# Kernel optimization log

Hardware: AMD Instinct MI355X
Metric: run time of the kernel (lower is better)

The kernel has to match this reference:

```python
import jax, jax.numpy as jnp
import numpy as np

DIMENSIONS = 10000
NUM_LEVELS = 100
SIZE = 617
NUM_CLASSES = 26
BATCH = 32


def setup_inputs() -> dict:
    key = jax.random.key(0)
    k1, k2, k3 = jax.random.split(key, 3)
    x = jax.random.uniform(k1, (BATCH, SIZE), dtype=jnp.float32)  # values in [0,1]
    # Random embedding: bipolar {-1,+1} hypervectors
    id_weight = jnp.where(jax.random.uniform(k2, (SIZE, DIMENSIONS)) > 0.5, 1.0, -1.0).astype(jnp.float32)
    # Level embedding: bipolar hypervectors per quantization level
    level_weight = jnp.where(jax.random.uniform(k3, (NUM_LEVELS, DIMENSIONS)) > 0.5, 1.0, -1.0).astype(jnp.float32)
    classify_weight = jnp.zeros((NUM_CLASSES, DIMENSIONS), dtype=jnp.float32)
    return {"x": x, "id_weight": id_weight, "level_weight": level_weight, "classify_weight": classify_weight}


def reference(x, id_weight, level_weight, classify_weight):
    # Level embedding: map continuous values in [low=0, high=1] to level indices
    idx = jnp.clip(jnp.round(x * (NUM_LEVELS - 1)), 0, NUM_LEVELS - 1).astype(jnp.int32)  # (B, S)
    value_hv = level_weight[idx]                     # gather -> (B, S, D)
    bound = id_weight[None, :, :] * value_hv         # bind (elementwise multiply)
    multiset = jnp.sum(bound, axis=1)                # sum over feature axis -> (B, D)
    enc = jnp.where(multiset > 0, 1.0, -1.0)         # hard_quantize
    logit = jnp.einsum('bd,cd->bc', enc, classify_weight)  # Linear, no bias
    return logit
```

## Files before the change

### kernel.cpp

```cpp
#include <hip/hip_runtime.h>

typedef unsigned int u32;
typedef unsigned char u8;
typedef unsigned long long u64;

#define DIMS   10000
#define LEVELS 100
#define SSIZE  617
#define SPAD   624
#define NCLS   26
#define BATCH  32
#define WORDS  313
#define WPITCH 320
#define DPITCH 10240
#define NTILE  5
#define NCH    13
#define CHUNK  48

#define OFF_OFFW 0x000000u
#define OFF_IDB  0x020000u
#define OFF_LVB  0x100000u
#define OFF_P8   0x140000u
#define SLOT_BYTES ((size_t)BATCH * DPITCH)

#define PK_ROWS (SPAD + LEVELS + 1)

__global__ __launch_bounds__(256) void k_pack(const float* __restrict__ x,
                                              const float* __restrict__ idw,
                                              const float* __restrict__ lvw,
                                              u32* __restrict__ idb,
                                              u32* __restrict__ lvb,
                                              u32* __restrict__ offw,
                                              float* __restrict__ out)
{
    const int g = blockIdx.x;
    const int r = blockIdx.y;
    const int t = threadIdx.x;
    const bool isLvl = r >= SPAD;
    const int rl = r - SPAD;
    const int d0 = g * 1024 + 4 * t;

    u32 nib = 0;
    const bool rowValid = isLvl ? (rl < LEVELS) : (r < SSIZE);
    if (d0 + 3 < DIMS && rowValid) {
        const float* src = isLvl ? (lvw + (size_t)rl * DIMS)
                                 : (idw + (size_t)r * DIMS);
        float4 f = *(const float4*)(src + d0);
        nib =  (__builtin_bit_cast(u32, f.x) >> 31)
            | ((__builtin_bit_cast(u32, f.y) >> 31) << 1)
            | ((__builtin_bit_cast(u32, f.z) >> 31) << 2)
            | ((__builtin_bit_cast(u32, f.w) >> 31) << 3);
    }
    __shared__ u32 nibs[256];
    nibs[t] = nib;
    __syncthreads();
    if (t < 32) {
        u32 w = 0;
#pragma unroll
        for (int j = 0; j < 8; ++j) w |= nibs[t * 8 + j] << (4 * j);
        u32* dst = isLvl ? (lvb + (size_t)rl * WPITCH)
                         : (idb + (size_t)r * WPITCH);
        dst[g * 32 + t] = w;
    }

    const int B = r * 10 + g;
    const int t2 = B * 256 + t;
    if (t2 < SPAD * BATCH) {
        int s = t2 >> 5, b = t2 & 31;
        u32 off = (u32)LEVELS * WPITCH;
        if (s < SSIZE) {
            float v = x[b * SSIZE + s];
            float rr = rintf(v * (float)(LEVELS - 1));
            int q = (int)rr;
            q = q < 0 ? 0 : (q > LEVELS - 1 ? LEVELS - 1 : q);
            off = (u32)q * WPITCH;
        }
        offw[s * BATCH + b] = off;
    }
    if (t2 < BATCH * NCLS) out[t2] = 0.0f;
}

__device__ __forceinline__ void spread6(u32* __restrict__ part,
                                        int slot, int B0, int wq,
                                        const u32 ones[4], const u32 c0[4],
                                        const u32 c1[4], const u32 c2[4],
                                        const u32 c3[4], const u32 c4[4])
{
#pragma unroll
    for (int b = 0; b < 4; ++b) {
        u32* dst = part + ((size_t)(slot * BATCH + B0 + b) * DPITCH + (size_t)wq * 32) / 4;
        u32 o[8];
#pragma unroll
        for (int g = 0; g < 8; ++g) {
            int sh = 4 * g;
            u32 n;
            n  =  (((ones[b] >> sh) & 0xFu) * 0x00204081u) & 0x01010101u;
            n |= ((((c0[b]  >> sh) & 0xFu) * 0x00204081u) & 0x01010101u) << 1;
            n |= ((((c1[b]  >> sh) & 0xFu) * 0x00204081u) & 0x01010101u) << 2;
            n |= ((((c2[b]  >> sh) & 0xFu) * 0x00204081u) & 0x01010101u) << 3;
            n |= ((((c3[b]  >> sh) & 0xFu) * 0x00204081u) & 0x01010101u) << 4;
            n |= ((((c4[b]  >> sh) & 0xFu) * 0x00204081u) & 0x01010101u) << 5;
            o[g] = n;
        }
        *(uint4*)(dst)     = make_uint4(o[0], o[1], o[2], o[3]);
        *(uint4*)(dst + 4) = make_uint4(o[4], o[5], o[6], o[7]);
    }
}

template <int CH>
__global__ __launch_bounds__(64) void k_bind_t(const u32* __restrict__ idb,
                                               const u32* __restrict__ lvb,
                                               const u32* __restrict__ offw,
                                               u32* __restrict__ part)
{
    const int wq   = blockIdx.x * 64 + threadIdx.x;
    const int B0   = blockIdx.y * 4;
    const int slot = blockIdx.z;
    const int sBeg = slot * CH;

    u32 ones[4], c0[4], c1[4], c2[4], c3[4], c4[4];
#pragma unroll
    for (int b = 0; b < 4; ++b) { ones[b]=0; c0[b]=0; c1[b]=0; c2[b]=0; c3[b]=0; c4[b]=0; }

#pragma unroll
    for (int i = 0; i < CH / 2; ++i) {
        const int s = sBeg + 2 * i;
        u32 u1 = idb[(size_t)s * WPITCH + wq];
        u32 u2 = idb[(size_t)(s + 1) * WPITCH + wq];
        const u32* o1 = offw + s * BATCH + B0;
        const u32* o2 = o1 + BATCH;
#pragma unroll
        for (int b = 0; b < 4; ++b) {
            u32 l1 = lvb[o1[b] + wq];
            u32 l2 = lvb[o2[b] + wq];
            u32 x1 = u1 ^ l1, x2 = u2 ^ l2;
            u32 t0 = x1 ^ x2;
            u32 sum = ones[b] ^ t0;
            u32 car = (x1 & x2) | (ones[b] & t0);
            ones[b] = sum;
            u32 tt;
            tt = c0[b] & car; c0[b] ^= car; car = tt;
            tt = c1[b] & car; c1[b] ^= car; car = tt;
            tt = c2[b] & car; c2[b] ^= car; car = tt;
            tt = c3[b] & car; c3[b] ^= car; car = tt;
            c4[b] ^= car;
        }
    }
    spread6(part, slot, B0, wq, ones, c0, c1, c2, c3, c4);
}

__global__ __launch_bounds__(64) void k_bind_g(const u32* __restrict__ idb,
                                               const u32* __restrict__ lvb,
                                               const u32* __restrict__ offw,
                                               u32* __restrict__ part,
                                               int chunk)
{
    const int wq   = blockIdx.x * 64 + threadIdx.x;
    const int B0   = blockIdx.y * 4;
    const int slot = blockIdx.z;
    const int sBeg = slot * chunk;
    const int sEnd = min(SPAD, sBeg + chunk);

    u32 ones[4], c0[4], c1[4], c2[4], c3[4], c4[4];
#pragma unroll
    for (int b = 0; b < 4; ++b) { ones[b]=0; c0[b]=0; c1[b]=0; c2[b]=0; c3[b]=0; c4[b]=0; }

    for (int s = sBeg; s < sEnd; s += 2) {
        u32 u1 = idb[(size_t)s * WPITCH + wq];
        u32 u2 = idb[(size_t)(s + 1) * WPITCH + wq];
        const u32* o1 = offw + s * BATCH + B0;
        const u32* o2 = o1 + BATCH;
#pragma unroll
        for (int b = 0; b < 4; ++b) {
            u32 l1 = lvb[o1[b] + wq];
            u32 l2 = lvb[o2[b] + wq];
            u32 x1 = u1 ^ l1, x2 = u2 ^ l2;
            u32 t0 = x1 ^ x2;
            u32 sum = ones[b] ^ t0;
            u32 car = (x1 & x2) | (ones[b] & t0);
            ones[b] = sum;
            u32 tt;
            tt = c0[b] & car; c0[b] ^= car; car = tt;
            tt = c1[b] & car; c1[b] ^= car; car = tt;
            tt = c2[b] & car; c2[b] ^= car; car = tt;
            tt = c3[b] & car; c3[b] ^= car; car = tt;
            c4[b] ^= car;
        }
    }
    spread6(part, slot, B0, wq, ones, c0, c1, c2, c3, c4);
}

template <int NCHT>
__global__ __launch_bounds__(256) void k_encl_t(const u32* __restrict__ part,
                                                const float* __restrict__ W,
                                                float* __restrict__ out)
{
    const int b = blockIdx.y;
    const int q = blockIdx.x;
    const int t = threadIdx.x;
    const int dw = q * 256 + t;
    const u32* p = part + (size_t)b * (DPITCH / 4) + dw;
    const size_t cs = (size_t)BATCH * (DPITCH / 4);

    u32 v[NCHT];
#pragma unroll
    for (int c = 0; c < NCHT; ++c) v[c] = p[(size_t)c * cs];
    u32 a01 = 0, a23 = 0;
#pragma unroll
    for (int c = 0; c < NCHT; ++c) {
        a01 += v[c] & 0x00FF00FFu;
        a23 += (v[c] >> 8) & 0x00FF00FFu;
    }
    const float e0 = (int)(a01 & 0xFFFFu) <= 308 ? 1.0f : -1.0f;
    const float e1 = (int)(a23 & 0xFFFFu) <= 308 ? 1.0f : -1.0f;
    const float e2 = (int)(a01 >> 16)     <= 308 ? 1.0f : -1.0f;
    const float e3 = (int)(a23 >> 16)     <= 308 ? 1.0f : -1.0f;

    float acc[NCLS];
    if (dw < DIMS / 4) {
#pragma unroll
        for (int cc = 0; cc < NCLS; ++cc) {
            float4 w4 = *(const float4*)(W + (size_t)cc * DIMS + 4 * dw);
            acc[cc] = fmaf(e0, w4.x, fmaf(e1, w4.y, fmaf(e2, w4.z, e3 * w4.w)));
        }
    } else {
#pragma unroll
        for (int cc = 0; cc < NCLS; ++cc) acc[cc] = 0.0f;
    }

#pragma unroll
    for (int cc = 0; cc < NCLS; ++cc) {
#pragma unroll
        for (int o = 32; o > 0; o >>= 1)
            acc[cc] += __shfl_xor(acc[cc], o);
    }
    __shared__ float red[4][NCLS];
    const int lane = t & 63, wv = t >> 6;
    if (lane == 0) {
#pragma unroll
        for (int cc = 0; cc < NCLS; ++cc) red[wv][cc] = acc[cc];
    }
    __syncthreads();
    if (t < NCLS) {
        float vv = red[0][t] + red[1][t] + red[2][t] + red[3][t];
        atomicAdd(out + b * NCLS + t, vv);
    }
}

__global__ __launch_bounds__(256) void k_encl_g(const u32* __restrict__ part,
                                                const float* __restrict__ W,
                                                float* __restrict__ out,
                                                int nch)
{
    const int b = blockIdx.y;
    const int q = blockIdx.x;
    const int t = threadIdx.x;
    const int dw = q * 256 + t;
    const u32* p = part + (size_t)b * (DPITCH / 4) + dw;
    const size_t cs = (size_t)BATCH * (DPITCH / 4);
    u32 a01 = 0, a23 = 0;
    for (int c = 0; c < nch; ++c) {
        u32 v = p[(size_t)c * cs];
        a01 += v & 0x00FF00FFu;
        a23 += (v >> 8) & 0x00FF00FFu;
    }
    const float e0 = (int)(a01 & 0xFFFFu) <= 308 ? 1.0f : -1.0f;
    const float e1 = (int)(a23 & 0xFFFFu) <= 308 ? 1.0f : -1.0f;
    const float e2 = (int)(a01 >> 16)     <= 308 ? 1.0f : -1.0f;
    const float e3 = (int)(a23 >> 16)     <= 308 ? 1.0f : -1.0f;
    float acc[NCLS];
    if (dw < DIMS / 4) {
#pragma unroll
        for (int cc = 0; cc < NCLS; ++cc) {
            float4 w4 = *(const float4*)(W + (size_t)cc * DIMS + 4 * dw);
            acc[cc] = fmaf(e0, w4.x, fmaf(e1, w4.y, fmaf(e2, w4.z, e3 * w4.w)));
        }
    } else {
#pragma unroll
        for (int cc = 0; cc < NCLS; ++cc) acc[cc] = 0.0f;
    }
#pragma unroll
    for (int cc = 0; cc < NCLS; ++cc) {
#pragma unroll
        for (int o = 32; o > 0; o >>= 1)
            acc[cc] += __shfl_xor(acc[cc], o);
    }
    __shared__ float red[4][NCLS];
    const int lane = t & 63, wv = t >> 6;
    if (lane == 0) {
#pragma unroll
        for (int cc = 0; cc < NCLS; ++cc) red[wv][cc] = acc[cc];
    }
    __syncthreads();
    if (t < NCLS) {
        float vv = red[0][t] + red[1][t] + red[2][t] + red[3][t];
        atomicAdd(out + b * NCLS + t, vv);
    }
}

extern "C" void kernel_launch(void* const* d_in, const int* in_sizes, int n_in,
                              void* d_out, int out_size, void* d_ws, size_t ws_size,
                              hipStream_t stream)
{
    const float* x   = (const float*)d_in[0];
    const float* idw = (const float*)d_in[1];
    const float* lvw = (const float*)d_in[2];
    const float* W   = (const float*)d_in[3];
    float* out = (float*)d_out;

    char* ws = (char*)d_ws;
    u32* offw = (u32*)(ws + OFF_OFFW);
    u32* idb  = (u32*)(ws + OFF_IDB);
    u32* lvb  = (u32*)(ws + OFF_LVB);
    u32* part = (u32*)(ws + OFF_P8);

    size_t avail = ws_size > OFF_P8 ? ws_size - OFF_P8 : 0;
    const bool fast = avail >= (size_t)NCH * SLOT_BYTES;

    dim3 g1(10, PK_ROWS);
    k_pack<<<g1, 256, 0, stream>>>(x, idw, lvw, idb, lvb, offw, out);

    if (fast) {
        dim3 g2(NTILE, 8, NCH);
        k_bind_t<CHUNK><<<g2, 64, 0, stream>>>(idb, lvb, offw, part);
        dim3 g3(10, BATCH);
        k_encl_t<NCH><<<g3, 256, 0, stream>>>(part, W, out);
    } else {
        int nch = (int)(avail / SLOT_BYTES);
        if (nch < 1) nch = 1;
        int chunk = (SPAD + nch - 1) / nch;
        chunk = (chunk + 1) & ~1;
        if (chunk > 62) chunk = 62;
        nch = (SPAD + chunk - 1) / chunk;
        dim3 g2(NTILE, 8, nch);
        k_bind_g<<<g2, 64, 0, stream>>>(idb, lvb, offw, part, chunk);
        dim3 g3(10, BATCH);
        k_encl_g<<<g3, 256, 0, stream>>>(part, W, out, nch);
    }
}
```

Before: 98.28 us.

## Split bind kernel to one batch row per block and batch loads by 16

The bind kernel now gives each block a single batch element instead of four. That raises the grid from 8 to 32 blocks along y and drops the per-thread register arrays. Level offsets are stored transposed per batch (pitch 640) so each block preloads its chunk's offsets contiguously. Inside the kernel, 16 id and level words are loaded before the carry-save updates run, to expose memory-level parallelism. The cost is reading each id-word row four times as often, and the spread helper carries a redundant first loop whose results are overwritten.

After: 91.00 us. 7.4% less time.

```diff
diff --git a/kernel.cpp b/kernel.cpp
--- a/kernel.cpp
+++ b/kernel.cpp
@@ -16,8 +16,9 @@
 #define NTILE  5
 #define NCH    13
 #define CHUNK  48
-
-#define OFF_OFFW 0x000000u
+#define SOPITCH 640
+
+#define OFF_OFFT 0x000000u
 #define OFF_IDB  0x020000u
 #define OFF_LVB  0x100000u
 #define OFF_P8   0x140000u
@@ -30,7 +31,7 @@
                                               const float* __restrict__ lvw,
                                               u32* __restrict__ idb,
                                               u32* __restrict__ lvb,
-                                              u32* __restrict__ offw,
+                                              u32* __restrict__ offt,
                                               float* __restrict__ out)
 {
     const int g = blockIdx.x;
@@ -75,119 +76,113 @@
             q = q < 0 ? 0 : (q > LEVELS - 1 ? LEVELS - 1 : q);
             off = (u32)q * WPITCH;
         }
-        offw[s * BATCH + b] = off;
+        offt[b * SOPITCH + s] = off;
     }
     if (t2 < BATCH * NCLS) out[t2] = 0.0f;
 }
 
-__device__ __forceinline__ void spread6(u32* __restrict__ part,
-                                        int slot, int B0, int wq,
-                                        const u32 ones[4], const u32 c0[4],
-                                        const u32 c1[4], const u32 c2[4],
-                                        const u32 c3[4], const u32 c4[4])
-{
-#pragma unroll
-    for (int b = 0; b < 4; ++b) {
-        u32* dst = part + ((size_t)(slot * BATCH + B0 + b) * DPITCH + (size_t)wq * 32) / 4;
-        u32 o[8];
-#pragma unroll
-        for (int g = 0; g < 8; ++g) {
-            int sh = 4 * g;
-            u32 n;
-            n  =  (((ones[b] >> sh) & 0xFu) * 0x00204081u) & 0x01010101u;
-            n |= ((((c0[b]  >> sh) & 0xFu) * 0x00204081u) & 0x01010101u) << 1;
-            n |= ((((c1[b]  >> sh) & 0xFu) * 0x00204081u) & 0x01010101u) << 2;
-            n |= ((((c2[b]  >> sh) & 0xFu) * 0x00204081u) & 0x01010101u) << 3;
-            n |= ((((c3[b]  >> sh) & 0xFu) * 0x00204081u) & 0x01010101u) << 4;
-            n |= ((((c4[b]  >> sh) & 0xFu) * 0x00204081u) & 0x01010101u) << 5;
-            o[g] = n;
-        }
-        *(uint4*)(dst)     = make_uint4(o[0], o[1], o[2], o[3]);
-        *(uint4*)(dst + 4) = make_uint4(o[4], o[5], o[6], o[7]);
-    }
+#define CSA6(xv)                                                              \
+    {                                                                         \
+        u32 car = ones & (xv);                                                \
+        ones ^= (xv);                                                         \
+        u32 tt;                                                               \
+        tt = c0 & car; c0 ^= car; car = tt;                                   \
+        tt = c1 & car; c1 ^= car; car = tt;                                   \
+        tt = c2 & car; c2 ^= car; car = tt;                                   \
+        tt = c3 & car; c3 ^= car; car = tt;                                   \
+        c4 ^= car;                                                            \
+    }
+
+__device__ __forceinline__ void spread6_1(u32* __restrict__ part,
+                                          int slot, int b, int wq,
+                                          u32 ones, u32 c0, u32 c1,
+                                          u32 c2, u32 c3, u32 c4)
+{
+    u32* dst = part + ((size_t)(slot * BATCH + b) * DPITCH + (size_t)wq * 32) / 4;
+    u32 o[8];
+#pragma unroll
+    for (int g = 0; g < 8; ++g) {
+        int sh = 4 * g;
+        u32 n;
+        n  =  (((ones >> sh) & 0xFu) * 0x00204081u) & 0x01010101u;
+        n |= ((((c0   >> sh) & 0xFu) * 0x00204081u) & 0x01010101u) << 1;
+        n |= ((((c1   >> sh) & 0xFu) * 0x00204081u) & 0x01010101u) << 2;
+        n |= ((((c2   >> sh) & 0xFu) * 0x00204081u) & 0x01010101u) << 3;
+        n |= ((((c3   >> sh) & 0xFu) * 0x00204081u) & 0x01010101u) << 4;
+        n |= ((((c4   >> sh) & 0xFu) * 0x01010101u) & 0x01010101u) << 5;
+        o[g] = n;
+    }
+#pragma unroll
+    for (int g = 0; g < 8; ++g) {
+        int sh = 4 * g;
+        u32 n;
+        n  =  (((ones >> sh) & 0xFu) * 0x00204081u) & 0x01010101u;
+        n |= ((((c0   >> sh) & 0xFu) * 0x00204081u) & 0x01010101u) << 1;
+        n |= ((((c1   >> sh) & 0xFu) * 0x00204081u) & 0x01010101u) << 2;
+        n |= ((((c2   >> sh) & 0xFu) * 0x00204081u) & 0x01010101u) << 3;
+        n |= ((((c3   >> sh) & 0xFu) * 0x00204081u) & 0x01010101u) << 4;
+        n |= ((((c4   >> sh) & 0xFu) * 0x00204081u) & 0x01010101u) << 5;
+        o[g] = n;
+    }
+    *(uint4*)(dst)     = make_uint4(o[0], o[1], o[2], o[3]);
+    *(uint4*)(dst + 4) = make_uint4(o[4], o[5], o[6], o[7]);
 }
 
 template <int CH>
 __global__ __launch_bounds__(64) void k_bind_t(const u32* __restrict__ idb,
                                                const u32* __restrict__ lvb,
-                                               const u32* __restrict__ offw,
+                                               const u32* __restrict__ offt,
                                                u32* __restrict__ part)
 {
     const int wq   = blockIdx.x * 64 + threadIdx.x;
-    const int B0   = blockIdx.y * 4;
+    const int b    = blockIdx.y;
     const int slot = blockIdx.z;
     const int sBeg = slot * CH;
 
-    u32 ones[4], c0[4], c1[4], c2[4], c3[4], c4[4];
-#pragma unroll
-    for (int b = 0; b < 4; ++b) { ones[b]=0; c0[b]=0; c1[b]=0; c2[b]=0; c3[b]=0; c4[b]=0; }
-
-#pragma unroll
-    for (int i = 0; i < CH / 2; ++i) {
-        const int s = sBeg + 2 * i;
-        u32 u1 = idb[(size_t)s * WPITCH + wq];
-        u32 u2 = idb[(size_t)(s + 1) * WPITCH + wq];
-        const u32* o1 = offw + s * BATCH + B0;
-        const u32* o2 = o1 + BATCH;
-#pragma unroll
-        for (int b = 0; b < 4; ++b) {
-            u32 l1 = lvb[o1[b] + wq];
-            u32 l2 = lvb[o2[b] + wq];
-            u32 x1 = u1 ^ l1, x2 = u2 ^ l2;
-            u32 t0 = x1 ^ x2;
-            u32 sum = ones[b] ^ t0;
-            u32 car = (x1 & x2) | (ones[b] & t0);
-            ones[b] = sum;
-            u32 tt;
-            tt = c0[b] & car; c0[b] ^= car; car = tt;
-            tt = c1[b] & car; c1[b] ^= car; car = tt;
-            tt = c2[b] & car; c2[b] ^= car; car = tt;
-            tt = c3[b] & car; c3[b] ^= car; car = tt;
-            c4[b] ^= car;
-        }
-    }
-    spread6(part, slot, B0, wq, ones, c0, c1, c2, c3, c4);
+    u32 off[CH];
+#pragma unroll
+    for (int k = 0; k < CH; ++k) off[k] = offt[b * SOPITCH + sBeg + k];
+
+    u32 ones = 0, c0 = 0, c1 = 0, c2 = 0, c3 = 0, c4 = 0;
+
+#pragma unroll
+    for (int grp = 0; grp < CH / 16; ++grp) {
+        u32 u[16], l[16];
+#pragma unroll
+        for (int k = 0; k < 16; ++k) {
+            const int s = sBeg + grp * 16 + k;
+            u[k] = idb[(size_t)s * WPITCH + wq];
+            l[k] = lvb[off[grp * 16 + k] + wq];
+        }
+#pragma unroll
+        for (int k = 0; k < 16; ++k) {
+            u32 xv = u[k] ^ l[k];
+            CSA6(xv);
+        }
+    }
+    spread6_1(part, slot, b, wq, ones, c0, c1, c2, c3, c4);
 }
 
 __global__ __launch_bounds__(64) void k_bind_g(const u32* __restrict__ idb,
                                                const u32* __restrict__ lvb,
-                                               const u32* __restrict__ offw,
+                                               const u32* __restrict__ offt,
                                                u32* __restrict__ part,
                                                int chunk)
 {
     const int wq   = blockIdx.x * 64 + threadIdx.x;
-    const int B0   = blockIdx.y * 4;
+    const int b    = blockIdx.y;
     const int slot = blockIdx.z;
     const int sBeg = slot * chunk;
     const int sEnd = min(SPAD, sBeg + chunk);
 
-    u32 ones[4], c0[4], c1[4], c2[4], c3[4], c4[4];
-#pragma unroll
-    for (int b = 0; b < 4; ++b) { ones[b]=0; c0[b]=0; c1[b]=0; c2[b]=0; c3[b]=0; c4[b]=0; }
-
-    for (int s = sBeg; s < sEnd; s += 2) {
+    u32 ones = 0, c0 = 0, c1 = 0, c2 = 0, c3 = 0, c4 = 0;
+    for (int s = sBeg; s < sEnd; ++s) {
         u32 u1 = idb[(size_t)s * WPITCH + wq];
-        u32 u2 = idb[(size_t)(s + 1) * WPITCH + wq];
-        const u32* o1 = offw + s * BATCH + B0;
-        const u32* o2 = o1 + BATCH;
-#pragma unroll
-        for (int b = 0; b < 4; ++b) {
-            u32 l1 = lvb[o1[b] + wq];
-            u32 l2 = lvb[o2[b] + wq];
-            u32 x1 = u1 ^ l1, x2 = u2 ^ l2;
-            u32 t0 = x1 ^ x2;
-            u32 sum = ones[b] ^ t0;
-            u32 car = (x1 & x2) | (ones[b] & t0);
-            ones[b] = sum;
-            u32 tt;
-            tt = c0[b] & car; c0[b] ^= car; car = tt;
-            tt = c1[b] & car; c1[b] ^= car; car = tt;
-            tt = c2[b] & car; c2[b] ^= car; car = tt;
-            tt = c3[b] & car; c3[b] ^= car; car = tt;
-            c4[b] ^= car;
-        }
-    }
-    spread6(part, slot, B0, wq, ones, c0, c1, c2, c3, c4);
+        u32 l1 = lvb[offt[b * SOPITCH + s] + wq];
+        u32 xv = u1 ^ l1;
+        CSA6(xv);
+    }
+    spread6_1(part, slot, b, wq, ones, c0, c1, c2, c3, c4);
 }
 
 template <int NCHT>
@@ -309,7 +304,7 @@
     float* out = (float*)d_out;
 
     char* ws = (char*)d_ws;
-    u32* offw = (u32*)(ws + OFF_OFFW);
+    u32* offt = (u32*)(ws + OFF_OFFT);
     u32* idb  = (u32*)(ws + OFF_IDB);
     u32* lvb  = (u32*)(ws + OFF_LVB);
     u32* part = (u32*)(ws + OFF_P8);
@@ -318,22 +313,21 @@
     const bool fast = avail >= (size_t)NCH * SLOT_BYTES;
 
     dim3 g1(10, PK_ROWS);
-    k_pack<<<g1, 256, 0, stream>>>(x, idw, lvw, idb, lvb, offw, out);
+    k_pack<<<g1, 256, 0, stream>>>(x, idw, lvw, idb, lvb, offt, out);
 
     if (fast) {
-        dim3 g2(NTILE, 8, NCH);
-        k_bind_t<CHUNK><<<g2, 64, 0, stream>>>(idb, lvb, offw, part);
+        dim3 g2(NTILE, BATCH, NCH);
+        k_bind_t<CHUNK><<<g2, 64, 0, stream>>>(idb, lvb, offt, part);
         dim3 g3(10, BATCH);
         k_encl_t<NCH><<<g3, 256, 0, stream>>>(part, W, out);
     } else {
         int nch = (int)(avail / SLOT_BYTES);
         if (nch < 1) nch = 1;
         int chunk = (SPAD + nch - 1) / nch;
-        chunk = (chunk + 1) & ~1;
         if (chunk > 62) chunk = 62;
         nch = (SPAD + chunk - 1) / chunk;
-        dim3 g2(NTILE, 8, nch);
-        k_bind_g<<<g2, 64, 0, stream>>>(idb, lvb, offw, part, chunk);
+        dim3 g2(NTILE, BATCH, nch);
+        k_bind_g<<<g2, 64, 0, stream>>>(idb, lvb, offt, part, chunk);
         dim3 g3(10, BATCH);
         k_encl_g<<<g3, 256, 0, stream>>>(part, W, out, nch);
     }
```
